# Performance work log

Hardware: AMD Instinct MI355X
Metric: run time of the kernel (lower is better)

Reference implementation:

```python
import jax, jax.numpy as jnp
import numpy as np

B, S, D, F, E = 2, 2048, 1024, 4096, 8
LN_EPS = 1e-5


def _xavier(key, shape, fan_in, fan_out):
    a = np.sqrt(6.0 / (fan_in + fan_out))
    return jax.random.uniform(key, shape, jnp.float32, -a, a)


def setup_inputs() -> dict:
    key = jax.random.key(0)
    ks = jax.random.split(key, 8)
    tgt = jax.random.normal(ks[0], (B, S, D), jnp.float32)
    router_w = _xavier(ks[1], (E, D), D, E)          # nn.Linear(d_model, num_experts).weight
    router_b = jnp.zeros((E,), jnp.float32)
    w1 = _xavier(ks[2], (E, D, F), D, F)             # expert first Linear, stored (in, out)
    b1 = jnp.zeros((E, F), jnp.float32)
    w2 = _xavier(ks[3], (E, F, D), F, D)             # expert second Linear
    b2 = jnp.zeros((E, D), jnp.float32)
    gamma = jnp.ones((D,), jnp.float32)
    beta = jnp.zeros((D,), jnp.float32)
    return {"tgt": tgt, "router_w": router_w, "router_b": router_b,
            "w1": w1, "b1": b1, "w2": w2, "b2": b2, "gamma": gamma, "beta": beta}


def reference(tgt, router_w, router_b, w1, b1, w2, b2, gamma, beta):
    # Router (computed then overwritten with a static one-hot on expert 0,
    # exactly as in the original forward_post)
    logits = jnp.einsum('bsd,ed->bse', tgt, router_w) + router_b
    rw = jax.nn.softmax(logits, axis=-1)
    rw = jnp.zeros_like(rw).at[..., 0].set(1.0)  # [B,S,E], one-hot expert 0

    # Dense all-expert FFN, vectorized over experts (same math as the python loop)
    h = jax.nn.relu(jnp.einsum('bsd,edf->besf', tgt, w1) + b1[None, :, None, :])
    eo = jnp.einsum('besf,efd->besd', h, w2) + b2[None, :, None, :]
    tgt2 = jnp.einsum('besd,bse->bsd', eo, rw)

    # Residual + post-LayerNorm (dropout = 0.0 -> identity)
    x = tgt + tgt2
    mean = jnp.mean(x, axis=-1, keepdims=True)
    var = jnp.mean(jnp.square(x - mean), axis=-1, keepdims=True)
    return (x - mean) * jax.lax.rsqrt(var + LN_EPS) * gamma + beta
```

## Files before the change

kernel.cpp:

```cpp
#include <hip/hip_runtime.h>
#include <hip/hip_bf16.h>
#include <stdint.h>

typedef unsigned short u16;
typedef __attribute__((ext_vector_type(8))) __bf16 bf16x8;
typedef __attribute__((ext_vector_type(4))) float f32x4;
typedef __attribute__((ext_vector_type(4))) unsigned short u16x4;
typedef __attribute__((ext_vector_type(8))) unsigned short u16x8;

#define LDS_AS __attribute__((address_space(3)))
#define GLB_AS __attribute__((address_space(1)))

__device__ __forceinline__ void async_copy16(const void* g, void* l) {
    __builtin_amdgcn_global_load_lds((const GLB_AS uint32_t*)g,
                                     (LDS_AS uint32_t*)l, 16, 0, 0);
}

__device__ __forceinline__ float bf2f(u16 u) {
    union { uint32_t i; float f; } x; x.i = (uint32_t)u << 16; return x.f;
}
__device__ __forceinline__ u16 f2bf(float f) {
    return __builtin_bit_cast(u16, __float2bfloat16(f));
}
__device__ __forceinline__ bool probe_bf16(const u16* gprobe) {
    return gprobe[0] == 0x3F80;
}
__device__ __forceinline__ float ldf(const void* p, size_t i, bool isb) {
    return isb ? bf2f(((const u16*)p)[i]) : ((const float*)p)[i];
}

__global__ __launch_bounds__(256)
void convert_kernel(const void* __restrict__ src, u16* __restrict__ dst, int n8,
                    const u16* __restrict__ gprobe) {
    const bool isb = probe_bf16(gprobe);
    int i = blockIdx.x * blockDim.x + threadIdx.x;
    if (i >= n8) return;
    u16x8 o;
    if (isb) {
        o = ((const u16x8*)src)[i];
    } else {
        const float* s = (const float*)src + (size_t)i * 8;
        #pragma unroll
        for (int j = 0; j < 8; ++j) o[j] = f2bf(s[j]);
    }
    ((u16x8*)dst)[i] = o;
}

__global__ __launch_bounds__(256)
void transpose_kernel(const void* __restrict__ src, u16* __restrict__ dst,
                      int R, int C, const u16* __restrict__ gprobe) {
    const bool isb = probe_bf16(gprobe);
    __shared__ u16 tile[32][33];
    const int nbx = C / 32;
    const int bx = blockIdx.x % nbx;
    const int by = blockIdx.x / nbx;
    const int x = threadIdx.x & 31;
    const int y = threadIdx.x >> 5;
    #pragma unroll
    for (int j = 0; j < 4; ++j) {
        int r = by * 32 + y + j * 8;
        size_t idx = (size_t)r * C + bx * 32 + x;
        tile[y + j * 8][x] = isb ? ((const u16*)src)[idx]
                                 : f2bf(((const float*)src)[idx]);
    }
    __syncthreads();
    #pragma unroll
    for (int j = 0; j < 4; ++j) {
        int cc = bx * 32 + y + j * 8;
        dst[(size_t)cc * R + by * 32 + x] = tile[x][y + j * 8];
    }
}

template<int MODE, int SPLITK>
__global__ __launch_bounds__(256, 4)
void gemm_kernel(const u16* __restrict__ A, const u16* __restrict__ Bt,
                 const void* __restrict__ bias, const void* __restrict__ resid,
                 u16* __restrict__ outB, float* __restrict__ outF,
                 int M, int N, int K, const u16* __restrict__ gprobe) {
    constexpr int BM = 128, BN = 128, BK = 32;
    __shared__ __attribute__((aligned(16))) u16 sA[2][BM * BK];
    __shared__ __attribute__((aligned(16))) u16 sB[2][BN * BK];

    const bool isb = probe_bf16(gprobe);
    const int t = threadIdx.x;
    const int lane = t & 63;
    const int wid = t >> 6;

    const int nwgb = gridDim.x / SPLITK;
    const int bid = blockIdx.x;
    const int ks = bid / nwgb;
    int tl = bid % nwgb;
    tl = (tl & 7) * (nwgb >> 3) + (tl >> 3);

    const int nbx = N / BN;
    const int bx = tl % nbx;
    const int by = tl / nbx;
    const long row0 = (long)by * BM;
    const long col0 = (long)bx * BN;

    const int wr = wid >> 1, wc = wid & 1;
    const int fr = lane & 15;
    const int kg = lane >> 4;

    const int Kc = K / SPLITK;
    const int kbeg = ks * Kc;
    const int nIter = Kc / BK;

    f32x4 acc[4][4] = {};

    auto stage = [&](int buf, int k0) {
        #pragma unroll
        for (int c = 0; c < 2; ++c) {
            int off16 = c * 256 + t;
            int row = off16 >> 2;
            int cb  = (off16 & 3) * 16;
            const char* ga = (const char*)(A  + (row0 + row) * (long)K + k0) + cb;
            const char* gb = (const char*)(Bt + (col0 + row) * (long)K + k0) + cb;
            async_copy16(ga, (char*)(&sA[buf][0]) + off16 * 16);
            async_copy16(gb, (char*)(&sB[buf][0]) + off16 * 16);
        }
    };

    stage(0, kbeg);
    asm volatile("s_waitcnt vmcnt(0)" ::: "memory");
    __syncthreads();

    for (int it = 0; it < nIter; ++it) {
        const int cur = it & 1;
        if (it + 1 < nIter) stage(cur ^ 1, kbeg + (it + 1) * BK);

        bf16x8 af[4], bfv[4];
        #pragma unroll
        for (int m = 0; m < 4; ++m)
            af[m] = *(const bf16x8*)&sA[cur][(wr * 64 + m * 16 + fr) * BK + kg * 8];
        #pragma unroll
        for (int n = 0; n < 4; ++n)
            bfv[n] = *(const bf16x8*)&sB[cur][(wc * 64 + n * 16 + fr) * BK + kg * 8];
        #pragma unroll
        for (int m = 0; m < 4; ++m)
            #pragma unroll
            for (int n = 0; n < 4; ++n)
                acc[m][n] = __builtin_amdgcn_mfma_f32_16x16x32_bf16(
                    af[m], bfv[n], acc[m][n], 0, 0, 0);

        asm volatile("s_waitcnt vmcnt(0)" ::: "memory");
        __syncthreads();
    }

    #pragma unroll
    for (int n = 0; n < 4; ++n) {
        long col = col0 + wc * 64 + n * 16 + fr;
        float bv = (MODE == 3) ? 0.f : ldf(bias, col, isb);
        #pragma unroll
        for (int m = 0; m < 4; ++m) {
            #pragma unroll
            for (int r = 0; r < 4; ++r) {
                long row = row0 + wr * 64 + m * 16 + kg * 4 + r;
                float v = acc[m][n][r] + bv;
                if (MODE == 1) {
                    v = v > 0.f ? v : 0.f;
                    outB[row * N + col] = f2bf(v);
                } else if (MODE == 2) {
                    v += ldf(resid, (size_t)row * N + col, isb);
                    outB[row * N + col] = f2bf(v);
                } else {
                    outF[((long)ks * M + row) * N + col] = v;
                }
            }
        }
    }
}

__global__ __launch_bounds__(256)
void ln_fused_kernel(const float* __restrict__ p0, const float* __restrict__ p1,
                     const void* __restrict__ bias, const void* __restrict__ resid,
                     const void* __restrict__ gamma, const void* __restrict__ beta,
                     void* __restrict__ out, const u16* __restrict__ gprobe) {
    const bool isb = probe_bf16(gprobe);
    const int row = blockIdx.x;
    const int t = threadIdx.x;
    const size_t base = (size_t)row * 1024 + t * 4;

    float4 a = *(const float4*)(p0 + base);
    float v[4] = { a.x, a.y, a.z, a.w };
    if (p1) {
        float4 b = *(const float4*)(p1 + base);
        v[0] += b.x; v[1] += b.y; v[2] += b.z; v[3] += b.w;
    }
    #pragma unroll
    for (int j = 0; j < 4; ++j)
        v[j] += ldf(bias, t * 4 + j, isb) + ldf(resid, base + j, isb);

    float s = 0.f, s2 = 0.f;
    #pragma unroll
    for (int j = 0; j < 4; ++j) { s += v[j]; s2 += v[j] * v[j]; }
    #pragma unroll
    for (int off = 32; off >= 1; off >>= 1) {
        s  += __shfl_xor(s, off, 64);
        s2 += __shfl_xor(s2, off, 64);
    }
    __shared__ float red[8];
    if ((t & 63) == 0) { red[t >> 6] = s; red[4 + (t >> 6)] = s2; }
    __syncthreads();
    s  = red[0] + red[1] + red[2] + red[3];
    s2 = red[4] + red[5] + red[6] + red[7];
    const float mean = s * (1.f / 1024.f);
    const float var  = s2 * (1.f / 1024.f) - mean * mean;
    const float rstd = rsqrtf(var + 1e-5f);

    float o[4];
    #pragma unroll
    for (int j = 0; j < 4; ++j) {
        float g = ldf(gamma, t * 4 + j, isb);
        float b = ldf(beta,  t * 4 + j, isb);
        o[j] = (v[j] - mean) * rstd * g + b;
    }
    if (isb) {
        u16x4 ov;
        #pragma unroll
        for (int j = 0; j < 4; ++j) ov[j] = f2bf(o[j]);
        ((u16x4*)((u16*)out))[base / 4] = ov;
    } else {
        float4 ov = { o[0], o[1], o[2], o[3] };
        *(float4*)((float*)out + base) = ov;
    }
}

__global__ __launch_bounds__(256)
void ln_kernel(const u16* __restrict__ X, const void* __restrict__ gamma,
               const void* __restrict__ beta, void* __restrict__ out,
               const u16* __restrict__ gprobe) {
    const bool isb = probe_bf16(gprobe);
    const int row = blockIdx.x;
    const int t = threadIdx.x;
    u16x4 xv = ((const u16x4*)(X + (size_t)row * 1024))[t];
    float v[4];
    #pragma unroll
    for (int j = 0; j < 4; ++j) v[j] = bf2f(xv[j]);
    float s = 0.f, s2 = 0.f;
    #pragma unroll
    for (int j = 0; j < 4; ++j) { s += v[j]; s2 += v[j] * v[j]; }
    #pragma unroll
    for (int off = 32; off >= 1; off >>= 1) {
        s  += __shfl_xor(s, off, 64);
        s2 += __shfl_xor(s2, off, 64);
    }
    __shared__ float red[8];
    if ((t & 63) == 0) { red[t >> 6] = s; red[4 + (t >> 6)] = s2; }
    __syncthreads();
    s  = red[0] + red[1] + red[2] + red[3];
    s2 = red[4] + red[5] + red[6] + red[7];
    const float mean = s * (1.f / 1024.f);
    const float var  = s2 * (1.f / 1024.f) - mean * mean;
    const float rstd = rsqrtf(var + 1e-5f);
    float o[4];
    #pragma unroll
    for (int j = 0; j < 4; ++j) {
        float g = ldf(gamma, t * 4 + j, isb);
        float b = ldf(beta,  t * 4 + j, isb);
        o[j] = (v[j] - mean) * rstd * g + b;
    }
    if (isb) {
        u16x4 ov;
        #pragma unroll
        for (int j = 0; j < 4; ++j) ov[j] = f2bf(o[j]);
        ((u16x4*)((u16*)out + (size_t)row * 1024))[t] = ov;
    } else {
        float4 ov = { o[0], o[1], o[2], o[3] };
        ((float4*)((float*)out + (size_t)row * 1024))[t] = ov;
    }
}

extern "C" void kernel_launch(void* const* d_in, const int* in_sizes, int n_in,
                              void* d_out, int out_size, void* d_ws, size_t ws_size,
                              hipStream_t stream) {
    constexpr int M = 4096;
    constexpr int D = 1024;
    constexpr int F = 4096;

    const void* tgt   = d_in[0];
    const void* w1    = d_in[3];
    const void* b1    = d_in[4];
    const void* w2    = d_in[5];
    const void* b2    = d_in[6];
    const void* gamma = d_in[7];
    const void* beta  = d_in[8];
    const u16* gprobe = (const u16*)gamma;

    char* ws = (char*)d_ws;
    u16* tgtB = (u16*)ws;
    u16* w1T  = (u16*)(ws + (8ull  << 20));
    u16* w2T  = (u16*)(ws + (16ull << 20));
    u16* H    = (u16*)(ws + (24ull << 20));
    const bool deep = ws_size >= (88ull << 20);
    float* P  = (float*)(ws + (56ull << 20));
    u16* X    = (u16*)(ws + (56ull << 20));

    convert_kernel<<<(M * D / 8 + 255) / 256, 256, 0, stream>>>(tgt, tgtB, M * D / 8, gprobe);
    transpose_kernel<<<(D / 32) * (F / 32), 256, 0, stream>>>(w1, w1T, D, F, gprobe);
    transpose_kernel<<<(F / 32) * (D / 32), 256, 0, stream>>>(w2, w2T, F, D, gprobe);

    gemm_kernel<1, 1><<<(F / 128) * (M / 128), 256, 0, stream>>>(
        tgtB, w1T, b1, nullptr, H, nullptr, M, F, D, gprobe);

    if (deep) {
        gemm_kernel<3, 2><<<2 * (D / 128) * (M / 128), 256, 0, stream>>>(
            H, w2T, nullptr, nullptr, nullptr, P, M, D, F, gprobe);
        ln_fused_kernel<<<M, 256, 0, stream>>>(
            P, P + (size_t)M * D, b2, tgt, gamma, beta, d_out, gprobe);
    } else {
        gemm_kernel<2, 1><<<(D / 128) * (M / 128), 256, 0, stream>>>(
            H, w2T, b2, tgt, X, nullptr, M, D, F, gprobe);
        ln_kernel<<<M, 256, 0, stream>>>(X, gamma, beta, d_out, gprobe);
    }
}
```

Baseline: 136.6 us.

## Replace 128x128 GEMM with 256x256 tiled, 8-wave pipelined kernel and split-K 4

Replaces the 128x128x32 GEMM with a 256x256x64 tile kernel using 8 waves. Each wave computes 128x64 of the output. LDS is laid out in MFMA fragment order, and the loads are staged in quarters interleaved with MFMA bursts under s_setprio and barriers. The second GEMM now uses split-K of 4 in place of 2, and the fused LayerNorm sums four fp32 partial slices, which needs a larger workspace. The aim is higher arithmetic intensity and overlap of global-to-LDS copies with matrix math. The costs are lower occupancy, more partial-sum traffic, and the deep path needing a larger workspace threshold.

New measurement: 142.6 us. 1.04x slower.

```diff
diff --git a/kernel.cpp b/kernel.cpp
--- a/kernel.cpp
+++ b/kernel.cpp
@@ -71,91 +71,107 @@
     }
 }
 
+#define DS_B(KS) { _Pragma("unroll") for (int n = 0; n < 4; ++n) \
+    bfv[n] = *(const bf16x8*)((const char*)&sB[cur][KS][0] + (wc*4+n)*1024 + lane*16); }
+#define DS_A(KS, MH) { _Pragma("unroll") for (int mm = 0; mm < 4; ++mm) \
+    af[mm] = *(const bf16x8*)((const char*)&sA[cur][KS][0] + (wr*8+(MH)*4+mm)*1024 + lane*16); }
+#define MFMA_Q(MH) { __builtin_amdgcn_s_setprio(1); \
+    _Pragma("unroll") for (int mm = 0; mm < 4; ++mm) \
+    _Pragma("unroll") for (int n = 0; n < 4; ++n) \
+        acc[(MH)*4+mm][n] = __builtin_amdgcn_mfma_f32_16x16x32_bf16(af[mm], bfv[n], acc[(MH)*4+mm][n], 0, 0, 0); \
+    __builtin_amdgcn_s_setprio(0); }
+
 template<int MODE, int SPLITK>
-__global__ __launch_bounds__(256, 4)
-void gemm_kernel(const u16* __restrict__ A, const u16* __restrict__ Bt,
-                 const void* __restrict__ bias, const void* __restrict__ resid,
-                 u16* __restrict__ outB, float* __restrict__ outF,
-                 int M, int N, int K, const u16* __restrict__ gprobe) {
-    constexpr int BM = 128, BN = 128, BK = 32;
-    __shared__ __attribute__((aligned(16))) u16 sA[2][BM * BK];
-    __shared__ __attribute__((aligned(16))) u16 sB[2][BN * BK];
-
-    const bool isb = probe_bf16(gprobe);
-    const int t = threadIdx.x;
-    const int lane = t & 63;
-    const int wid = t >> 6;
+__global__ __launch_bounds__(512, 2)
+void gemm256_kernel(const u16* __restrict__ A, const u16* __restrict__ Bt,
+                    const void* __restrict__ bias, const void* __restrict__ resid,
+                    u16* __restrict__ outB, float* __restrict__ outF,
+                    int M, int N, int K, const u16* __restrict__ gprobe) {
+    __shared__ __attribute__((aligned(16))) u16 sA[2][2][8192];
+    __shared__ __attribute__((aligned(16))) u16 sB[2][2][8192];
+
+    const bool isb = probe_bf16(gprobe);
+    const int t = threadIdx.x, lane = t & 63, w = t >> 6;
+    const int wr = w >> 2, wc = w & 3;
+    const int fr = lane & 15, kg = lane >> 4;
 
     const int nwgb = gridDim.x / SPLITK;
-    const int bid = blockIdx.x;
-    const int ks = bid / nwgb;
-    int tl = bid % nwgb;
+    const int slc = blockIdx.x / nwgb;
+    int tl = blockIdx.x % nwgb;
     tl = (tl & 7) * (nwgb >> 3) + (tl >> 3);
-
-    const int nbx = N / BN;
-    const int bx = tl % nbx;
-    const int by = tl / nbx;
-    const long row0 = (long)by * BM;
-    const long col0 = (long)bx * BN;
-
-    const int wr = wid >> 1, wc = wid & 1;
-    const int fr = lane & 15;
-    const int kg = lane >> 4;
-
+    const int nbx = N / 256;
+    const long row0 = (long)(tl / nbx) * 256;
+    const long col0 = (long)(tl % nbx) * 256;
     const int Kc = K / SPLITK;
-    const int kbeg = ks * Kc;
-    const int nIter = Kc / BK;
-
-    f32x4 acc[4][4] = {};
-
-    auto stage = [&](int buf, int k0) {
+    const long kbeg = (long)slc * Kc;
+    const int nk = Kc / 64;
+
+    f32x4 acc[8][4] = {};
+
+    const long ldb = (long)K * 2;
+    const char* Agb = (const char*)A;
+    const char* Bgb = (const char*)Bt;
+
+    auto stageT = [&](const char* gb, long r0, char* ldsbase, long k0, int ksr) {
         #pragma unroll
         for (int c = 0; c < 2; ++c) {
-            int off16 = c * 256 + t;
-            int row = off16 >> 2;
-            int cb  = (off16 & 3) * 16;
-            const char* ga = (const char*)(A  + (row0 + row) * (long)K + k0) + cb;
-            const char* gb = (const char*)(Bt + (col0 + row) * (long)K + k0) + cb;
-            async_copy16(ga, (char*)(&sA[buf][0]) + off16 * 16);
-            async_copy16(gb, (char*)(&sB[buf][0]) + off16 * 16);
+            const int G = w * 2 + c;
+            const char* src = gb + (r0 + G * 16 + fr) * ldb + (k0 + ksr * 32) * 2 + kg * 16;
+            async_copy16(src, ldsbase + G * 1024 + lane * 16);
         }
     };
 
-    stage(0, kbeg);
-    asm volatile("s_waitcnt vmcnt(0)" ::: "memory");
-    __syncthreads();
-
-    for (int it = 0; it < nIter; ++it) {
-        const int cur = it & 1;
-        if (it + 1 < nIter) stage(cur ^ 1, kbeg + (it + 1) * BK);
-
+    stageT(Agb, row0, (char*)&sA[0][0][0], kbeg, 0);
+    stageT(Bgb, col0, (char*)&sB[0][0][0], kbeg, 0);
+    stageT(Agb, row0, (char*)&sA[0][1][0], kbeg, 1);
+    stageT(Bgb, col0, (char*)&sB[0][1][0], kbeg, 1);
+    asm volatile("s_waitcnt vmcnt(4)" ::: "memory");
+    __builtin_amdgcn_s_barrier();
+
+    for (int kt = 0; kt < nk; ++kt) {
+        const int cur = kt & 1, nb = cur ^ 1;
+        const bool st = (kt + 1 < nk);
+        const long nk0 = kbeg + (long)(kt + 1) * 64;
         bf16x8 af[4], bfv[4];
-        #pragma unroll
-        for (int m = 0; m < 4; ++m)
-            af[m] = *(const bf16x8*)&sA[cur][(wr * 64 + m * 16 + fr) * BK + kg * 8];
-        #pragma unroll
-        for (int n = 0; n < 4; ++n)
-            bfv[n] = *(const bf16x8*)&sB[cur][(wc * 64 + n * 16 + fr) * BK + kg * 8];
-        #pragma unroll
-        for (int m = 0; m < 4; ++m)
-            #pragma unroll
-            for (int n = 0; n < 4; ++n)
-                acc[m][n] = __builtin_amdgcn_mfma_f32_16x16x32_bf16(
-                    af[m], bfv[n], acc[m][n], 0, 0, 0);
-
-        asm volatile("s_waitcnt vmcnt(0)" ::: "memory");
-        __syncthreads();
+
+        DS_B(0); DS_A(0, 0);
+        if (st) stageT(Agb, row0, (char*)&sA[nb][0][0], nk0, 0);
+        __builtin_amdgcn_s_barrier();
+        MFMA_Q(0);
+        __builtin_amdgcn_s_barrier();
+
+        DS_A(0, 1);
+        if (st) stageT(Bgb, col0, (char*)&sB[nb][0][0], nk0, 0);
+        __builtin_amdgcn_s_barrier();
+        MFMA_Q(1);
+        if (st) asm volatile("s_waitcnt vmcnt(4)" ::: "memory");
+        else    asm volatile("s_waitcnt vmcnt(0)" ::: "memory");
+        __builtin_amdgcn_s_barrier();
+
+        DS_B(1); DS_A(1, 0);
+        if (st) stageT(Agb, row0, (char*)&sA[nb][1][0], nk0, 1);
+        __builtin_amdgcn_s_barrier();
+        MFMA_Q(0);
+        __builtin_amdgcn_s_barrier();
+
+        DS_A(1, 1);
+        if (st) stageT(Bgb, col0, (char*)&sB[nb][1][0], nk0, 1);
+        __builtin_amdgcn_s_barrier();
+        MFMA_Q(1);
+        if (st) asm volatile("s_waitcnt vmcnt(4)" ::: "memory");
+        else    asm volatile("s_waitcnt vmcnt(0)" ::: "memory");
+        __builtin_amdgcn_s_barrier();
     }
 
     #pragma unroll
     for (int n = 0; n < 4; ++n) {
-        long col = col0 + wc * 64 + n * 16 + fr;
+        const long col = col0 + wc * 64 + n * 16 + fr;
         float bv = (MODE == 3) ? 0.f : ldf(bias, col, isb);
         #pragma unroll
-        for (int m = 0; m < 4; ++m) {
+        for (int m = 0; m < 8; ++m) {
             #pragma unroll
             for (int r = 0; r < 4; ++r) {
-                long row = row0 + wr * 64 + m * 16 + kg * 4 + r;
+                const long row = row0 + wr * 128 + m * 16 + kg * 4 + r;
                 float v = acc[m][n][r] + bv;
                 if (MODE == 1) {
                     v = v > 0.f ? v : 0.f;
@@ -164,7 +180,7 @@
                     v += ldf(resid, (size_t)row * N + col, isb);
                     outB[row * N + col] = f2bf(v);
                 } else {
-                    outF[((long)ks * M + row) * N + col] = v;
+                    outF[((long)slc * M + row) * N + col] = v;
                 }
             }
         }
@@ -172,20 +188,20 @@
 }
 
 __global__ __launch_bounds__(256)
-void ln_fused_kernel(const float* __restrict__ p0, const float* __restrict__ p1,
-                     const void* __restrict__ bias, const void* __restrict__ resid,
-                     const void* __restrict__ gamma, const void* __restrict__ beta,
-                     void* __restrict__ out, const u16* __restrict__ gprobe) {
+void ln_fused4_kernel(const float* __restrict__ P, long sliceStride,
+                      const void* __restrict__ bias, const void* __restrict__ resid,
+                      const void* __restrict__ gamma, const void* __restrict__ beta,
+                      void* __restrict__ out, const u16* __restrict__ gprobe) {
     const bool isb = probe_bf16(gprobe);
     const int row = blockIdx.x;
     const int t = threadIdx.x;
     const size_t base = (size_t)row * 1024 + t * 4;
 
-    float4 a = *(const float4*)(p0 + base);
-    float v[4] = { a.x, a.y, a.z, a.w };
-    if (p1) {
-        float4 b = *(const float4*)(p1 + base);
-        v[0] += b.x; v[1] += b.y; v[2] += b.z; v[3] += b.w;
+    float v[4] = {0.f, 0.f, 0.f, 0.f};
+    #pragma unroll
+    for (int s = 0; s < 4; ++s) {
+        float4 a = *(const float4*)(P + s * sliceStride + base);
+        v[0] += a.x; v[1] += a.y; v[2] += a.z; v[3] += a.w;
     }
     #pragma unroll
     for (int j = 0; j < 4; ++j)
@@ -292,7 +308,7 @@
     u16* w1T  = (u16*)(ws + (8ull  << 20));
     u16* w2T  = (u16*)(ws + (16ull << 20));
     u16* H    = (u16*)(ws + (24ull << 20));
-    const bool deep = ws_size >= (88ull << 20);
+    const bool deep = ws_size >= (121ull << 20);
     float* P  = (float*)(ws + (56ull << 20));
     u16* X    = (u16*)(ws + (56ull << 20));
 
@@ -300,16 +316,16 @@
     transpose_kernel<<<(D / 32) * (F / 32), 256, 0, stream>>>(w1, w1T, D, F, gprobe);
     transpose_kernel<<<(F / 32) * (D / 32), 256, 0, stream>>>(w2, w2T, F, D, gprobe);
 
-    gemm_kernel<1, 1><<<(F / 128) * (M / 128), 256, 0, stream>>>(
+    gemm256_kernel<1, 1><<<(M / 256) * (F / 256), 512, 0, stream>>>(
         tgtB, w1T, b1, nullptr, H, nullptr, M, F, D, gprobe);
 
     if (deep) {
-        gemm_kernel<3, 2><<<2 * (D / 128) * (M / 128), 256, 0, stream>>>(
+        gemm256_kernel<3, 4><<<4 * (M / 256) * (D / 256), 512, 0, stream>>>(
             H, w2T, nullptr, nullptr, nullptr, P, M, D, F, gprobe);
-        ln_fused_kernel<<<M, 256, 0, stream>>>(
-            P, P + (size_t)M * D, b2, tgt, gamma, beta, d_out, gprobe);
+        ln_fused4_kernel<<<M, 256, 0, stream>>>(
+            P, (long)M * D, b2, tgt, gamma, beta, d_out, gprobe);
     } else {
-        gemm_kernel<2, 1><<<(D / 128) * (M / 128), 256, 0, stream>>>(
+        gemm256_kernel<2, 1><<<(M / 256) * (D / 256), 512, 0, stream>>>(
             H, w2T, b2, tgt, X, nullptr, M, D, F, gprobe);
         ln_kernel<<<M, 256, 0, stream>>>(X, gamma, beta, d_out, gprobe);
     }
```

## Fuse prep kernels into one launch and pipeline GEMM loads with partial waitcnt

Applied to the files above, without the earlier changes.

Merges the tgt conversion and the two weight transposes into a single prep kernel launch, dispatching on block index, so two kernel launches go away. Inside the GEMM the staging addresses are precomputed once. The prefetch wait now uses vmcnt(4), so only the current buffer's loads must land and the next tile's async copies stay in flight during the MFMAs. Raw s_barrier replaces __syncthreads, which relies on careful ordering for LDS correctness.

New measurement: 130.8 us. 4.2% less time.

```diff
diff --git a/kernel.cpp b/kernel.cpp
--- a/kernel.cpp
+++ b/kernel.cpp
@@ -30,30 +30,34 @@
 }
 
 __global__ __launch_bounds__(256)
-void convert_kernel(const void* __restrict__ src, u16* __restrict__ dst, int n8,
-                    const u16* __restrict__ gprobe) {
-    const bool isb = probe_bf16(gprobe);
-    int i = blockIdx.x * blockDim.x + threadIdx.x;
-    if (i >= n8) return;
-    u16x8 o;
-    if (isb) {
-        o = ((const u16x8*)src)[i];
-    } else {
-        const float* s = (const float*)src + (size_t)i * 8;
-        #pragma unroll
-        for (int j = 0; j < 8; ++j) o[j] = f2bf(s[j]);
-    }
-    ((u16x8*)dst)[i] = o;
-}
-
-__global__ __launch_bounds__(256)
-void transpose_kernel(const void* __restrict__ src, u16* __restrict__ dst,
-                      int R, int C, const u16* __restrict__ gprobe) {
+void prep_kernel(const void* __restrict__ tgt, u16* __restrict__ tgtB,
+                 const void* __restrict__ w1, u16* __restrict__ w1T,
+                 const void* __restrict__ w2, u16* __restrict__ w2T,
+                 const u16* __restrict__ gprobe) {
+    constexpr int D = 1024, F = 4096;
     const bool isb = probe_bf16(gprobe);
     __shared__ u16 tile[32][33];
+    const int bid = blockIdx.x;
+
+    if (bid < 2048) {
+        const int i = bid * 256 + threadIdx.x;
+        u16x8 o;
+        if (isb) {
+            o = ((const u16x8*)tgt)[i];
+        } else {
+            const float* s = (const float*)tgt + (size_t)i * 8;
+            #pragma unroll
+            for (int j = 0; j < 8; ++j) o[j] = f2bf(s[j]);
+        }
+        ((u16x8*)tgtB)[i] = o;
+        return;
+    }
+    const void* src; u16* dst; int R, C, b;
+    if (bid < 6144) { src = w1; dst = w1T; R = D; C = F; b = bid - 2048; }
+    else            { src = w2; dst = w2T; R = F; C = D; b = bid - 6144; }
     const int nbx = C / 32;
-    const int bx = blockIdx.x % nbx;
-    const int by = blockIdx.x / nbx;
+    const int bx = b % nbx;
+    const int by = b / nbx;
     const int x = threadIdx.x & 31;
     const int y = threadIdx.x >> 5;
     #pragma unroll
@@ -103,39 +107,43 @@
     const int kg = lane >> 4;
 
     const int Kc = K / SPLITK;
-    const int kbeg = ks * Kc;
+    const long kbeg = (long)ks * Kc;
     const int nIter = Kc / BK;
 
     f32x4 acc[4][4] = {};
 
-    auto stage = [&](int buf, int k0) {
-        #pragma unroll
-        for (int c = 0; c < 2; ++c) {
-            int off16 = c * 256 + t;
-            int row = off16 >> 2;
-            int cb  = (off16 & 3) * 16;
-            const char* ga = (const char*)(A  + (row0 + row) * (long)K + k0) + cb;
-            const char* gb = (const char*)(Bt + (col0 + row) * (long)K + k0) + cb;
-            async_copy16(ga, (char*)(&sA[buf][0]) + off16 * 16);
-            async_copy16(gb, (char*)(&sB[buf][0]) + off16 * 16);
+    const long ldb = (long)K * 2;
+    const int srow = t >> 2, scb = (t & 3) * 16;
+    const char* gA0 = (const char*)A  + (row0 + srow) * ldb + kbeg * 2 + scb;
+    const char* gB0 = (const char*)Bt + (col0 + srow) * ldb + kbeg * 2 + scb;
+    const long half = 64 * ldb;
+
+    auto stage = [&](int buf, int it) {
+        const long ko = (long)it * (BK * 2);
+        async_copy16(gA0 + ko,        (char*)&sA[buf][0] + t * 16);
+        async_copy16(gA0 + half + ko, (char*)&sA[buf][0] + 4096 + t * 16);
+        async_copy16(gB0 + ko,        (char*)&sB[buf][0] + t * 16);
+        async_copy16(gB0 + half + ko, (char*)&sB[buf][0] + 4096 + t * 16);
+    };
+
+    stage(0, 0);
+    int buf = 0;
+    for (int it = 0; it < nIter; ++it) {
+        if (it + 1 < nIter) {
+            stage(buf ^ 1, it + 1);
+            asm volatile("s_waitcnt vmcnt(4)" ::: "memory");
+        } else {
+            asm volatile("s_waitcnt vmcnt(0)" ::: "memory");
         }
-    };
-
-    stage(0, kbeg);
-    asm volatile("s_waitcnt vmcnt(0)" ::: "memory");
-    __syncthreads();
-
-    for (int it = 0; it < nIter; ++it) {
-        const int cur = it & 1;
-        if (it + 1 < nIter) stage(cur ^ 1, kbeg + (it + 1) * BK);
+        asm volatile("s_barrier" ::: "memory");
 
         bf16x8 af[4], bfv[4];
         #pragma unroll
         for (int m = 0; m < 4; ++m)
-            af[m] = *(const bf16x8*)&sA[cur][(wr * 64 + m * 16 + fr) * BK + kg * 8];
+            af[m] = *(const bf16x8*)&sA[buf][(wr * 64 + m * 16 + fr) * BK + kg * 8];
         #pragma unroll
         for (int n = 0; n < 4; ++n)
-            bfv[n] = *(const bf16x8*)&sB[cur][(wc * 64 + n * 16 + fr) * BK + kg * 8];
+            bfv[n] = *(const bf16x8*)&sB[buf][(wc * 64 + n * 16 + fr) * BK + kg * 8];
         #pragma unroll
         for (int m = 0; m < 4; ++m)
             #pragma unroll
@@ -143,8 +151,8 @@
                 acc[m][n] = __builtin_amdgcn_mfma_f32_16x16x32_bf16(
                     af[m], bfv[n], acc[m][n], 0, 0, 0);
 
-        asm volatile("s_waitcnt vmcnt(0)" ::: "memory");
-        __syncthreads();
+        asm volatile("s_barrier" ::: "memory");
+        buf ^= 1;
     }
 
     #pragma unroll
@@ -296,9 +304,7 @@
     float* P  = (float*)(ws + (56ull << 20));
     u16* X    = (u16*)(ws + (56ull << 20));
 
-    convert_kernel<<<(M * D / 8 + 255) / 256, 256, 0, stream>>>(tgt, tgtB, M * D / 8, gprobe);
-    transpose_kernel<<<(D / 32) * (F / 32), 256, 0, stream>>>(w1, w1T, D, F, gprobe);
-    transpose_kernel<<<(F / 32) * (D / 32), 256, 0, stream>>>(w2, w2T, F, D, gprobe);
+    prep_kernel<<<10240, 256, 0, stream>>>(tgt, tgtB, w1, w1T, w2, w2T, gprobe);
 
     gemm_kernel<1, 1><<<(F / 128) * (M / 128), 256, 0, stream>>>(
         tgtB, w1T, b1, nullptr, H, nullptr, M, F, D, gprobe);
```
